# Performance work log

Hardware: AMD Instinct MI355X
Metric: run time of the kernel (lower is better)

Reference implementation:

```python
import jax, jax.numpy as jnp
import numpy as np

D = 128          # data_dim
H = 512          # hidden_dim
K = 10           # num_bins
BATCH = 32768
BOUND = 5.0
MINW = 1e-3
MINH = 1e-3
MIND = 1e-3
MASK = np.array([1.0] * (D // 2) + [0.0] * (D // 2), dtype=np.float32)
TIDX = np.where(MASK == 0)[0]  # transformed dims (static)


def _rqs_forward(x, uw, uh, ud):
    # x: [B, T]; uw/uh: [B, T, K]; ud: [B, T, K-1]
    w = jax.nn.softmax(uw, axis=-1)
    w = MINW + (1.0 - MINW * K) * w
    cw = jnp.pad(jnp.cumsum(w, axis=-1), ((0, 0), (0, 0), (1, 0)))
    cw = 2.0 * BOUND * cw - BOUND
    cw = cw.at[..., 0].set(-BOUND).at[..., -1].set(BOUND)
    w = cw[..., 1:] - cw[..., :-1]

    h = jax.nn.softmax(uh, axis=-1)
    h = MINH + (1.0 - MINH * K) * h
    ch = jnp.pad(jnp.cumsum(h, axis=-1), ((0, 0), (0, 0), (1, 0)))
    ch = 2.0 * BOUND * ch - BOUND
    ch = ch.at[..., 0].set(-BOUND).at[..., -1].set(BOUND)
    h = ch[..., 1:] - ch[..., :-1]

    d = MIND + jax.nn.softplus(ud)
    d = jnp.pad(d, ((0, 0), (0, 0), (1, 1)), constant_values=1.0)  # [B,T,K+1]

    inside = (x >= -BOUND) & (x <= BOUND)
    xc = jnp.clip(x, -BOUND, BOUND)  # avoid NaN for outside values

    # searchsorted(cw, x, right=True) - 1, clamped to [0, K-1]
    bin_idx = jnp.clip(jnp.sum(cw <= xc[..., None], axis=-1) - 1, 0, K - 1)

    def gat(a, idx):
        return jnp.take_along_axis(a, idx[..., None], axis=-1)[..., 0]

    wk = gat(w, bin_idx)
    cwk = gat(cw, bin_idx)
    hk = gat(h, bin_idx)
    chk = gat(ch, bin_idx)
    dk = gat(d, bin_idx)
    dk1 = gat(d, bin_idx + 1)

    theta = (xc - cwk) / wk
    s = hk / wk
    tm = theta * (1.0 - theta)
    den = s + (dk + dk1 - 2.0 * s) * tm
    num = hk * (s * theta * theta + dk * tm)
    y = chk + num / den
    ld = jnp.log(s * s * (dk1 * theta * theta + 2.0 * s * tm + dk * (1.0 - theta) ** 2)) - 2.0 * jnp.log(den)

    y = jnp.where(inside, y, x)
    ld = jnp.where(inside, ld, 0.0)
    return y, ld


def setup_inputs() -> dict:
    key = jax.random.key(0)
    ks = jax.random.split(key, 7)
    out_dim = D * (3 * K - 1)
    return {
        "z": jax.random.normal(ks[0], (BATCH, D), dtype=jnp.float32) * 2.0,
        "W1": jax.random.normal(ks[1], (H, D), dtype=jnp.float32) * 0.05,
        "b1": jnp.zeros((H,), dtype=jnp.float32),
        "W2": jax.random.normal(ks[2], (H, H), dtype=jnp.float32) * 0.05,
        "b2": jnp.zeros((H,), dtype=jnp.float32),
        "W3": jax.random.normal(ks[3], (out_dim, H), dtype=jnp.float32) * 0.05,
        "b3": jnp.zeros((out_dim,), dtype=jnp.float32),
    }


def reference(z, W1, b1, W2, b2, W3, b3):
    mask = jnp.asarray(MASK)
    z_a = z * mask
    hdn = jax.nn.relu(z_a @ W1.T + b1)
    hdn = jax.nn.relu(hdn @ W2.T + b2)
    p = (hdn @ W3.T + b3).reshape(-1, D, 3 * K - 1)
    uw, uh, ud = jnp.split(p, [K, 2 * K], axis=-1)

    zb = z[:, TIDX]
    xb, ld = _rqs_forward(zb, uw[:, TIDX], uh[:, TIDX], ud[:, TIDX])

    x = z.at[:, TIDX].set(xb)
    logdet = jnp.sum(ld, axis=1)
    x = jnp.where(jnp.isnan(x) | jnp.isinf(x), 0.0, x)
    logdet = jnp.where(jnp.isnan(logdet) | jnp.isinf(logdet), 0.0, logdet)
    return x, logdet
```

## Files before the change

### kernel.cpp

```cpp
#include <hip/hip_runtime.h>
#include <cmath>

#define BATCH 32768
#define DIM   128
#define HID   512
#define NPAD  2048

typedef __attribute__((ext_vector_type(8))) _Float16 half8;
typedef __attribute__((ext_vector_type(8))) short   short8v;
typedef __attribute__((ext_vector_type(4))) float   f32x4;
typedef unsigned short u16;


__device__ __forceinline__ u16 f2h(float f) {
  _Float16 h = (_Float16)f;
  union { _Float16 h; u16 u; } v; v.h = h; return v.u;
}

__device__ __forceinline__ void async16(const void* g, void* l) {
  __builtin_amdgcn_global_load_lds(
      (const __attribute__((address_space(1))) void*)g,
      (__attribute__((address_space(3))) void*)l, 16, 0, 0);
}

__device__ __forceinline__ int xcd_swz(int bid, int nwg) {
  int cpx = nwg >> 3;
  return (bid & 7) * cpx + (bid >> 3);
}


__global__ __launch_bounds__(256) void prep_za_v7(const float* __restrict__ z, u16* __restrict__ zh) {
  int id = blockIdx.x * 256 + threadIdx.x;
  int l = id & 63;
  int mb = (id >> 6) & 2047;
  int kt = id >> 17;
  int r = mb * 16 + (l & 15);
  int k0 = kt * 32 + ((l >> 4) << 3);
  const float* src = z + (size_t)r * DIM + k0;
  short8v H;
#pragma unroll
  for (int j = 0; j < 8; ++j) H[j] = (short)f2h(src[j]);
  *(short8v*)(zh + (size_t)id * 8) = H;
}

__global__ __launch_bounds__(256) void prep_w12_v7(const float* __restrict__ W1, const float* __restrict__ W2,
                                                   u16* __restrict__ W1h, u16* __restrict__ W2h) {
  int id = blockIdx.x * 256 + threadIdx.x;
  if (id < 4096) {
    int l = id & 63, mb = (id >> 6) & 31, kt = id >> 11;
    int r = mb * 16 + (l & 15);
    int k0 = kt * 32 + ((l >> 4) << 3);
    const float* src = W1 + (size_t)r * DIM + k0;
    short8v H;
#pragma unroll
    for (int j = 0; j < 8; ++j) H[j] = (short)f2h(src[j]);
    *(short8v*)(W1h + (size_t)id * 8) = H;
  } else {
    int id2 = id - 4096;
    int l = id2 & 63, mb = (id2 >> 6) & 31, kt = id2 >> 11;
    int r = mb * 16 + (l & 15);
    int k0 = kt * 32 + ((l >> 4) << 3);
    const float* src = W2 + (size_t)r * HID + k0;
    short8v H;
#pragma unroll
    for (int j = 0; j < 8; ++j) H[j] = (short)f2h(src[j]);
    *(short8v*)(W2h + (size_t)id2 * 8) = H;
  }
}

__global__ __launch_bounds__(256) void prep_w3_v7(const float* __restrict__ W3, u16* __restrict__ W3h) {
  int id = blockIdx.x * 256 + threadIdx.x;
  int l = id & 63, mb = (id >> 6) & 127, kt = id >> 13;
  int n = mb * 16 + (l & 15);
  int k0 = kt * 32 + ((l >> 4) << 3);
  int g = n >> 5, kk = n & 31;
  short8v H;
  if (kk < 29) {
    const float* src = W3 + ((size_t)((g + 64) * 29 + kk)) * HID + k0;
#pragma unroll
    for (int j = 0; j < 8; ++j) H[j] = (short)f2h(src[j]);
  } else {
#pragma unroll
    for (int j = 0; j < 8; ++j) H[j] = 0;
  }
  *(short8v*)(W3h + (size_t)id * 8) = H;
}

__global__ __launch_bounds__(256) void prep_b3_v7(const float* __restrict__ b3, float* __restrict__ b3p) {
  int n = blockIdx.x * 256 + threadIdx.x;
  int g = n >> 5, kk = n & 31;
  b3p[n] = (kk < 29) ? b3[(g + 64) * 29 + kk] : 0.f;
}


__device__ __forceinline__ void stage4(const u16* __restrict__ A, const u16* __restrict__ B,
                                       size_t ab, size_t bb, u16* Lb, int t) {
  async16(A + ab + t * 8,         Lb + t * 8);
  async16(A + ab + (t + 256) * 8, Lb + (t + 256) * 8);
  async16(B + bb + t * 8,         Lb + 4096 + t * 8);
  async16(B + bb + (t + 256) * 8, Lb + 4096 + (t + 256) * 8);
}

__device__ __forceinline__ void compute_v7(const u16* Lb, int lane, int wr, int wc, f32x4 acc[4][4]) {
  half8 a[4], b[4];
#pragma unroll
  for (int mf = 0; mf < 4; ++mf)
    a[mf] = *(const half8*)(Lb + ((wr * 4 + mf) * 64 + lane) * 8);
#pragma unroll
  for (int nf = 0; nf < 4; ++nf)
    b[nf] = *(const half8*)(Lb + 4096 + ((wc * 4 + nf) * 64 + lane) * 8);
#pragma unroll
  for (int mf = 0; mf < 4; ++mf)
#pragma unroll
    for (int nf = 0; nf < 4; ++nf)
      acc[mf][nf] = __builtin_amdgcn_mfma_f32_16x16x32_f16(a[mf], b[nf], acc[mf][nf], 0, 0, 0);
}

__device__ __forceinline__ void gemm_mainloop_v7(
    const u16* __restrict__ A, const u16* __restrict__ B,
    int nkt, int a_rb0, int a_rs16, int b_rb0, int b_rs16,
    u16* LDS, f32x4 acc[4][4]) {
  const int t = threadIdx.x;
  const int lane = t & 63;
  const int wv = t >> 6;
  const int wr = wv >> 1, wc = wv & 1;
  const size_t aStep = (size_t)a_rs16 * 512;
  const size_t bStep = (size_t)b_rs16 * 512;
  size_t ab = (size_t)a_rb0 * 512;
  size_t bb = (size_t)b_rb0 * 512;

  stage4(A, B, ab, bb, LDS, t);
  stage4(A, B, ab + aStep, bb + bStep, LDS + 8192, t);

  for (int kt = 0; kt < nkt; ++kt) {
    if (kt + 2 < nkt) {
      stage4(A, B, ab + 2 * aStep, bb + 2 * bStep, LDS + ((kt + 2) & 3) * 8192, t);
      asm volatile("s_waitcnt vmcnt(8)" ::: "memory");
    } else if (kt + 1 < nkt) {
      asm volatile("s_waitcnt vmcnt(4)" ::: "memory");
    } else {
      asm volatile("s_waitcnt vmcnt(0)" ::: "memory");
    }
    __builtin_amdgcn_s_barrier();
    __builtin_amdgcn_sched_barrier(0);
    compute_v7(LDS + (kt & 3) * 8192, lane, wr, wc, acc);
    ab += aStep; bb += bStep;
  }
}


__global__ __launch_bounds__(256) void gemm_relu_v7(
    const u16* __restrict__ A, const u16* __restrict__ B,
    const float* __restrict__ bias, u16* __restrict__ C,
    int nkt, int a_rs16) {
  __shared__ __align__(16) u16 LDS[32768];
  const int bid = xcd_swz(blockIdx.x, gridDim.x);
  const int nt = bid & 3;
  const int mt = bid >> 2;
  const int m0 = mt << 7, n0 = nt << 7;
  f32x4 zero = {0.f, 0.f, 0.f, 0.f};
  f32x4 acc[4][4];
#pragma unroll
  for (int i = 0; i < 4; ++i)
#pragma unroll
    for (int j = 0; j < 4; ++j) acc[i][j] = zero;

  gemm_mainloop_v7(A, B, nkt, m0 >> 4, a_rs16, n0 >> 4, 32, LDS, acc);

  const int lane = threadIdx.x & 63;
  const int wv = threadIdx.x >> 6;
  const int wr = wv >> 1, wc = wv & 1;
#pragma unroll
  for (int mf = 0; mf < 4; ++mf) {
#pragma unroll
    for (int nf = 0; nf < 4; ++nf) {
      int col = n0 + wc * 64 + nf * 16 + (lane & 15);
      float bv = bias[col];
#pragma unroll
      for (int r = 0; r < 4; ++r) {
        int row = m0 + wr * 64 + mf * 16 + (lane >> 4) * 4 + r;
        float v = fmaxf(acc[mf][nf][r] + bv, 0.f);
        int ktO = col >> 5, mbO = row >> 4;
        int lO = (row & 15) | (((col >> 3) & 3) << 4);
        int jO = col & 7;
        size_t off = (((size_t)ktO * (BATCH >> 4) + mbO) * 64 + lO) * 8 + jO;
        C[off] = f2h(v);
      }
    }
  }
}


__device__ __forceinline__ void rqs(float xin, const float uw[10], const float uh[10], const float ud9[9],
                                    float& yv, float& ldv) {
  float mw = uw[0];
#pragma unroll
  for (int i = 1; i < 10; ++i) mw = fmaxf(mw, uw[i]);
  float ew[10]; float sw = 0.f;
#pragma unroll
  for (int i = 0; i < 10; ++i) { ew[i] = __expf(uw[i] - mw); sw += ew[i]; }
  float invw = 0.99f / sw;
  float cw[11]; cw[0] = -5.f;
  {
    float run = 0.f;
#pragma unroll
    for (int i = 0; i < 10; ++i) { run += 0.001f + invw * ew[i]; cw[i + 1] = 10.f * run - 5.f; }
  }
  cw[10] = 5.f;
  float mh = uh[0];
#pragma unroll
  for (int i = 1; i < 10; ++i) mh = fmaxf(mh, uh[i]);
  float eh[10]; float sh = 0.f;
#pragma unroll
  for (int i = 0; i < 10; ++i) { eh[i] = __expf(uh[i] - mh); sh += eh[i]; }
  float invh = 0.99f / sh;
  float ch[11]; ch[0] = -5.f;
  {
    float run = 0.f;
#pragma unroll
    for (int i = 0; i < 10; ++i) { run += 0.001f + invh * eh[i]; ch[i + 1] = 10.f * run - 5.f; }
  }
  ch[10] = 5.f;
  float dv[11]; dv[0] = 1.f; dv[10] = 1.f;
#pragma unroll
  for (int i = 0; i < 9; ++i) {
    float x = ud9[i];
    float sp = fmaxf(x, 0.f) + __logf(1.f + __expf(-fabsf(x)));
    dv[i + 1] = 0.001f + sp;
  }

  float xc = fminf(fmaxf(xin, -5.f), 5.f);
  int b = 0;
#pragma unroll
  for (int j = 1; j <= 10; ++j) b += (cw[j] <= xc) ? 1 : 0;
  b = (b > 9) ? 9 : b;

  float wk = cw[1] - cw[0], cwk = cw[0], hk = ch[1] - ch[0], chk = ch[0], dk = dv[0], dk1 = dv[1];
#pragma unroll
  for (int j = 1; j < 10; ++j) {
    if (j == b) { wk = cw[j + 1] - cw[j]; cwk = cw[j]; hk = ch[j + 1] - ch[j]; chk = ch[j]; dk = dv[j]; dk1 = dv[j + 1]; }
  }

  float th = (xc - cwk) / wk;
  float sr = hk / wk;
  float omth = 1.f - th;
  float tm = th * omth;
  float den = sr + (dk + dk1 - 2.f * sr) * tm;
  float num = hk * (sr * th * th + dk * tm);
  float y = chk + num / den;
  float ld = __logf(sr * sr * (dk1 * th * th + 2.f * sr * tm + dk * omth * omth)) - 2.f * __logf(den);
  bool inside = (xin >= -5.f) && (xin <= 5.f);
  yv = inside ? y : xin;
  ldv = inside ? ld : 0.f;
  if (!isfinite(yv)) yv = 0.f;
}


__global__ __launch_bounds__(256) void gemm3_spline_v7(
    const u16* __restrict__ A, const u16* __restrict__ B,
    const float* __restrict__ b3p, const float* __restrict__ z,
    float* __restrict__ xout, float* __restrict__ partial) {
  __shared__ __align__(16) char SMEM[65536];
  u16* LDS = (u16*)SMEM;
  float (*PT)[135] = (float(*)[135])SMEM;
  const int bid = xcd_swz(blockIdx.x, gridDim.x);
  const int nt = bid & 15;
  const int mt = bid >> 4;
  const int m0 = mt << 7, n0 = nt << 7;
  f32x4 zero = {0.f, 0.f, 0.f, 0.f};
  f32x4 acc[4][4];
#pragma unroll
  for (int i = 0; i < 4; ++i)
#pragma unroll
    for (int j = 0; j < 4; ++j) acc[i][j] = zero;

  gemm_mainloop_v7(A, B, 16, m0 >> 4, BATCH >> 4, n0 >> 4, NPAD >> 4, LDS, acc);

  const int t = threadIdx.x;
  const int lane = t & 63;
  const int wv = t >> 6;
  const int wr = wv >> 1, wc = wv & 1;
  const int gb = n0 >> 5;

  for (int p = 0; p < 2; ++p) {
    __syncthreads();
    if (wr == p) {
#pragma unroll
      for (int mf = 0; mf < 4; ++mf)
#pragma unroll
        for (int nf = 0; nf < 4; ++nf)
#pragma unroll
          for (int r = 0; r < 4; ++r) {
            int cl = wc * 64 + nf * 16 + (lane & 15);
            PT[mf * 16 + (lane >> 4) * 4 + r][(cl >> 5) * 33 + (cl & 31)] = acc[mf][nf][r];
          }
    }
    __syncthreads();

    const int rl = t >> 2;
    const int g = t & 3;
    const int row = p * 64 + rl;
    const int grow = m0 + row;
    const float* pr = &PT[rl][g * 33];
    const float* bb = b3p + n0 + g * 32;
    float uw[10], uh[10], ud9[9];
#pragma unroll
    for (int i = 0; i < 10; ++i) uw[i] = pr[i] + bb[i];
#pragma unroll
    for (int i = 0; i < 10; ++i) uh[i] = pr[10 + i] + bb[10 + i];
#pragma unroll
    for (int i = 0; i < 9; ++i) ud9[i] = pr[20 + i] + bb[20 + i];

    float xin = z[(long)grow * DIM + 64 + gb + g];
    float yv, ldv;
    rqs(xin, uw, uh, ud9, yv, ldv);

    xout[(long)grow * DIM + 64 + gb + g] = yv;

    float s = ldv;
    s += __shfl_down(s, 1);
    s += __shfl_down(s, 2);
    if (g == 0) partial[(long)nt * BATCH + grow] = s;
  }
}


__global__ __launch_bounds__(256) void copy_first_v7(const float* __restrict__ z, float* __restrict__ xout) {
  int id = blockIdx.x * 256 + threadIdx.x;
  int m = id >> 4, c4 = id & 15;
  const float4 v = *(const float4*)(z + (long)m * DIM + c4 * 4);
  *(float4*)(xout + (long)m * DIM + c4 * 4) = v;
}

__global__ __launch_bounds__(256) void reduce_ld_v7(const float* __restrict__ partial, float* __restrict__ ldout) {
  int row = blockIdx.x * 256 + threadIdx.x;
  float s = 0.f;
#pragma unroll
  for (int i = 0; i < 16; ++i) s += partial[(long)i * BATCH + row];
  if (!isfinite(s)) s = 0.f;
  ldout[row] = s;
}


extern "C" void kernel_launch(void* const* d_in, const int* in_sizes, int n_in,
                              void* d_out, int out_size, void* d_ws, size_t ws_size,
                              hipStream_t stream) {
  const float* z  = (const float*)d_in[0];
  const float* W1 = (const float*)d_in[1];
  const float* b1 = (const float*)d_in[2];
  const float* W2 = (const float*)d_in[3];
  const float* b2 = (const float*)d_in[4];
  const float* W3 = (const float*)d_in[5];
  const float* b3 = (const float*)d_in[6];
  float* xout  = (float*)d_out;
  float* ldout = xout + (size_t)BATCH * DIM;

  char* ws = (char*)d_ws;
  u16* W1h = (u16*)ws;  ws += (size_t)512 * 64 * 2;
  u16* W2h = (u16*)ws;  ws += (size_t)512 * 512 * 2;
  u16* W3h = (u16*)ws;  ws += (size_t)NPAD * HID * 2;
  float* b3p = (float*)ws; ws += (size_t)NPAD * 4;
  u16* zah  = (u16*)ws;
  float* part = (float*)ws; ws += (size_t)BATCH * 64 * 2;
  u16* h1h = (u16*)ws;  ws += (size_t)BATCH * HID * 2;
  u16* h2h = (u16*)ws;  ws += (size_t)BATCH * HID * 2;

  prep_za_v7 <<<(2 * 2048 * 64) / 256, 256, 0, stream>>>(z, zah);
  prep_w12_v7<<<(4096 + 32768) / 256, 256, 0, stream>>>(W1, W2, W1h, W2h);
  prep_w3_v7 <<<(16 * 128 * 64) / 256, 256, 0, stream>>>(W3, W3h);
  prep_b3_v7 <<<NPAD / 256, 256, 0, stream>>>(b3, b3p);

  gemm_relu_v7<<<(BATCH / 128) * 4, 256, 0, stream>>>(zah, W1h, b1, h1h, 2, BATCH >> 4);
  gemm_relu_v7<<<(BATCH / 128) * 4, 256, 0, stream>>>(h1h, W2h, b2, h2h, 16, BATCH >> 4);
  gemm3_spline_v7<<<(BATCH / 128) * (NPAD / 128), 256, 0, stream>>>(h2h, W3h, b3p, z, xout, part);

  copy_first_v7<<<(BATCH * 16) / 256, 256, 0, stream>>>(z, xout);
  reduce_ld_v7<<<BATCH / 256, 256, 0, stream>>>(part, ldout);
}
```

Measured before the change: 182.6 us.

## Load GEMM B fragments directly to registers, halve LDS, merge prep kernels

```diff
diff --git a/kernel.cpp b/kernel.cpp
--- a/kernel.cpp
+++ b/kernel.cpp
@@ -29,96 +29,77 @@
 }
 
 
-__global__ __launch_bounds__(256) void prep_za_v7(const float* __restrict__ z, u16* __restrict__ zh) {
-  int id = blockIdx.x * 256 + threadIdx.x;
-  int l = id & 63;
-  int mb = (id >> 6) & 2047;
-  int kt = id >> 17;
-  int r = mb * 16 + (l & 15);
-  int k0 = kt * 32 + ((l >> 4) << 3);
-  const float* src = z + (size_t)r * DIM + k0;
-  short8v H;
-#pragma unroll
-  for (int j = 0; j < 8; ++j) H[j] = (short)f2h(src[j]);
-  *(short8v*)(zh + (size_t)id * 8) = H;
-}
-
-__global__ __launch_bounds__(256) void prep_w12_v7(const float* __restrict__ W1, const float* __restrict__ W2,
-                                                   u16* __restrict__ W1h, u16* __restrict__ W2h) {
-  int id = blockIdx.x * 256 + threadIdx.x;
-  if (id < 4096) {
-    int l = id & 63, mb = (id >> 6) & 31, kt = id >> 11;
+__global__ __launch_bounds__(256) void prep_all_v8(
+    const float* __restrict__ z, const float* __restrict__ W1, const float* __restrict__ W2,
+    const float* __restrict__ W3, const float* __restrict__ b3,
+    u16* __restrict__ zh, u16* __restrict__ W1h, u16* __restrict__ W2h,
+    u16* __restrict__ W3h, float* __restrict__ b3p) {
+  const int bid = blockIdx.x;
+  if (bid < 1024) {
+    int id = bid * 256 + threadIdx.x;
+    int l = id & 63, mb = (id >> 6) & 2047, kt = id >> 17;
     int r = mb * 16 + (l & 15);
     int k0 = kt * 32 + ((l >> 4) << 3);
-    const float* src = W1 + (size_t)r * DIM + k0;
+    const float* src = z + (size_t)r * DIM + k0;
     short8v H;
 #pragma unroll
     for (int j = 0; j < 8; ++j) H[j] = (short)f2h(src[j]);
-    *(short8v*)(W1h + (size_t)id * 8) = H;
+    *(short8v*)(zh + (size_t)id * 8) = H;
+  } else if (bid < 1168) {
+    int id = (bid - 1024) * 256 + threadIdx.x;
+    if (id < 4096) {
+      int l = id & 63, mb = (id >> 6) & 31, kt = id >> 11;
+      int r = mb * 16 + (l & 15);
+      int k0 = kt * 32 + ((l >> 4) << 3);
+      const float* src = W1 + (size_t)r * DIM + k0;
+      short8v H;
+#pragma unroll
+      for (int j = 0; j < 8; ++j) H[j] = (short)f2h(src[j]);
+      *(short8v*)(W1h + (size_t)id * 8) = H;
+    } else {
+      int id2 = id - 4096;
+      int l = id2 & 63, mb = (id2 >> 6) & 31, kt = id2 >> 11;
+      int r = mb * 16 + (l & 15);
+      int k0 = kt * 32 + ((l >> 4) << 3);
+      const float* src = W2 + (size_t)r * HID + k0;
+      short8v H;
+#pragma unroll
+      for (int j = 0; j < 8; ++j) H[j] = (short)f2h(src[j]);
+      *(short8v*)(W2h + (size_t)id2 * 8) = H;
+    }
+  } else if (bid < 1680) {
+    int id = (bid - 1168) * 256 + threadIdx.x;
+    int l = id & 63, mb = (id >> 6) & 127, kt = id >> 13;
+    int n = mb * 16 + (l & 15);
+    int k0 = kt * 32 + ((l >> 4) << 3);
+    int g = n >> 5, kk = n & 31;
+    short8v H;
+    if (kk < 29) {
+      const float* src = W3 + ((size_t)((g + 64) * 29 + kk)) * HID + k0;
+#pragma unroll
+      for (int j = 0; j < 8; ++j) H[j] = (short)f2h(src[j]);
+    } else {
+#pragma unroll
+      for (int j = 0; j < 8; ++j) H[j] = 0;
+    }
+    *(short8v*)(W3h + (size_t)id * 8) = H;
   } else {
-    int id2 = id - 4096;
-    int l = id2 & 63, mb = (id2 >> 6) & 31, kt = id2 >> 11;
-    int r = mb * 16 + (l & 15);
-    int k0 = kt * 32 + ((l >> 4) << 3);
-    const float* src = W2 + (size_t)r * HID + k0;
-    short8v H;
-#pragma unroll
-    for (int j = 0; j < 8; ++j) H[j] = (short)f2h(src[j]);
-    *(short8v*)(W2h + (size_t)id2 * 8) = H;
-  }
-}
-
-__global__ __launch_bounds__(256) void prep_w3_v7(const float* __restrict__ W3, u16* __restrict__ W3h) {
-  int id = blockIdx.x * 256 + threadIdx.x;
-  int l = id & 63, mb = (id >> 6) & 127, kt = id >> 13;
-  int n = mb * 16 + (l & 15);
-  int k0 = kt * 32 + ((l >> 4) << 3);
-  int g = n >> 5, kk = n & 31;
-  short8v H;
-  if (kk < 29) {
-    const float* src = W3 + ((size_t)((g + 64) * 29 + kk)) * HID + k0;
-#pragma unroll
-    for (int j = 0; j < 8; ++j) H[j] = (short)f2h(src[j]);
-  } else {
-#pragma unroll
-    for (int j = 0; j < 8; ++j) H[j] = 0;
-  }
-  *(short8v*)(W3h + (size_t)id * 8) = H;
-}
-
-__global__ __launch_bounds__(256) void prep_b3_v7(const float* __restrict__ b3, float* __restrict__ b3p) {
-  int n = blockIdx.x * 256 + threadIdx.x;
-  int g = n >> 5, kk = n & 31;
-  b3p[n] = (kk < 29) ? b3[(g + 64) * 29 + kk] : 0.f;
-}
-
-
-__device__ __forceinline__ void stage4(const u16* __restrict__ A, const u16* __restrict__ B,
-                                       size_t ab, size_t bb, u16* Lb, int t) {
+    int n = (bid - 1680) * 256 + threadIdx.x;
+    int g = n >> 5, kk = n & 31;
+    b3p[n] = (kk < 29) ? b3[(g + 64) * 29 + kk] : 0.f;
+  }
+}
+
+
+__device__ __forceinline__ void stageA_v8(const u16* __restrict__ A, size_t ab, u16* Lb, int t) {
   async16(A + ab + t * 8,         Lb + t * 8);
   async16(A + ab + (t + 256) * 8, Lb + (t + 256) * 8);
-  async16(B + bb + t * 8,         Lb + 4096 + t * 8);
-  async16(B + bb + (t + 256) * 8, Lb + 4096 + (t + 256) * 8);
-}
-
-__device__ __forceinline__ void compute_v7(const u16* Lb, int lane, int wr, int wc, f32x4 acc[4][4]) {
-  half8 a[4], b[4];
-#pragma unroll
-  for (int mf = 0; mf < 4; ++mf)
-    a[mf] = *(const half8*)(Lb + ((wr * 4 + mf) * 64 + lane) * 8);
-#pragma unroll
-  for (int nf = 0; nf < 4; ++nf)
-    b[nf] = *(const half8*)(Lb + 4096 + ((wc * 4 + nf) * 64 + lane) * 8);
-#pragma unroll
-  for (int mf = 0; mf < 4; ++mf)
-#pragma unroll
-    for (int nf = 0; nf < 4; ++nf)
-      acc[mf][nf] = __builtin_amdgcn_mfma_f32_16x16x32_f16(a[mf], b[nf], acc[mf][nf], 0, 0, 0);
-}
-
-__device__ __forceinline__ void gemm_mainloop_v7(
+}
+
+template<int NKT>
+__device__ __forceinline__ void gemm_mainloop_v8(
     const u16* __restrict__ A, const u16* __restrict__ B,
-    int nkt, int a_rb0, int a_rs16, int b_rb0, int b_rs16,
+    int a_rb0, int a_rs16, int b_rb0, int b_rs16,
     u16* LDS, f32x4 acc[4][4]) {
   const int t = threadIdx.x;
   const int lane = t & 63;
@@ -126,34 +107,48 @@
   const int wr = wv >> 1, wc = wv & 1;
   const size_t aStep = (size_t)a_rs16 * 512;
   const size_t bStep = (size_t)b_rs16 * 512;
-  size_t ab = (size_t)a_rb0 * 512;
-  size_t bb = (size_t)b_rb0 * 512;
-
-  stage4(A, B, ab, bb, LDS, t);
-  stage4(A, B, ab + aStep, bb + bStep, LDS + 8192, t);
-
-  for (int kt = 0; kt < nkt; ++kt) {
-    if (kt + 2 < nkt) {
-      stage4(A, B, ab + 2 * aStep, bb + 2 * bStep, LDS + ((kt + 2) & 3) * 8192, t);
-      asm volatile("s_waitcnt vmcnt(8)" ::: "memory");
-    } else if (kt + 1 < nkt) {
-      asm volatile("s_waitcnt vmcnt(4)" ::: "memory");
-    } else {
-      asm volatile("s_waitcnt vmcnt(0)" ::: "memory");
-    }
+  const size_t ab0 = (size_t)a_rb0 * 512;
+  const u16* Bbase = B + (((size_t)(b_rb0 + wc * 4)) * 64 + lane) * 8;
+
+  half8 breg[2][4];
+#pragma unroll
+  for (int nf = 0; nf < 4; ++nf)
+    breg[0][nf] = *(const half8*)(Bbase + nf * 512);
+  stageA_v8(A, ab0, LDS, t);
+  if (NKT > 1) stageA_v8(A, ab0 + aStep, LDS + 4096, t);
+
+#pragma unroll
+  for (int kt = 0; kt < NKT; ++kt) {
+    if (kt + 1 < NKT) {
+#pragma unroll
+      for (int nf = 0; nf < 4; ++nf)
+        breg[(kt + 1) & 1][nf] = *(const half8*)(Bbase + (size_t)(kt + 1) * bStep + nf * 512);
+    }
+    if (kt + 2 < NKT)
+      stageA_v8(A, ab0 + (size_t)(kt + 2) * aStep, LDS + ((kt + 2) & 3) * 4096, t);
+    if (kt + 2 < NKT)      asm volatile("s_waitcnt vmcnt(8)" ::: "memory");
+    else if (kt + 1 < NKT) asm volatile("s_waitcnt vmcnt(6)" ::: "memory");
+    else                   asm volatile("s_waitcnt vmcnt(0)" ::: "memory");
     __builtin_amdgcn_s_barrier();
     __builtin_amdgcn_sched_barrier(0);
-    compute_v7(LDS + (kt & 3) * 8192, lane, wr, wc, acc);
-    ab += aStep; bb += bStep;
-  }
-}
-
-
-__global__ __launch_bounds__(256) void gemm_relu_v7(
+    half8 a[4];
+#pragma unroll
+    for (int mf = 0; mf < 4; ++mf)
+      a[mf] = *(const half8*)(LDS + (kt & 3) * 4096 + ((wr * 4 + mf) * 64 + lane) * 8);
+#pragma unroll
+    for (int mf = 0; mf < 4; ++mf)
+#pragma unroll
+      for (int nf = 0; nf < 4; ++nf)
+        acc[mf][nf] = __builtin_amdgcn_mfma_f32_16x16x32_f16(a[mf], breg[kt & 1][nf], acc[mf][nf], 0, 0, 0);
+  }
+}
+
+
+template<int NKT>
+__global__ __launch_bounds__(256, 3) void gemm_relu_v8(
     const u16* __restrict__ A, const u16* __restrict__ B,
-    const float* __restrict__ bias, u16* __restrict__ C,
-    int nkt, int a_rs16) {
-  __shared__ __align__(16) u16 LDS[32768];
+    const float* __restrict__ bias, u16* __restrict__ C, int a_rs16) {
+  __shared__ __align__(16) u16 LDS[16384];
   const int bid = xcd_swz(blockIdx.x, gridDim.x);
   const int nt = bid & 3;
   const int mt = bid >> 2;
@@ -165,7 +160,7 @@
 #pragma unroll
     for (int j = 0; j < 4; ++j) acc[i][j] = zero;
 
-  gemm_mainloop_v7(A, B, nkt, m0 >> 4, a_rs16, n0 >> 4, 32, LDS, acc);
+  gemm_mainloop_v8<NKT>(A, B, m0 >> 4, a_rs16, n0 >> 4, 32, LDS, acc);
 
   const int lane = threadIdx.x & 63;
   const int wv = threadIdx.x >> 6;
@@ -256,13 +251,13 @@
 }
 
 
-__global__ __launch_bounds__(256) void gemm3_spline_v7(
+__global__ __launch_bounds__(256, 3) void gemm3_spline_v8(
     const u16* __restrict__ A, const u16* __restrict__ B,
     const float* __restrict__ b3p, const float* __restrict__ z,
     float* __restrict__ xout, float* __restrict__ partial) {
-  __shared__ __align__(16) char SMEM[65536];
+  __shared__ __align__(16) char SMEM[33792];
   u16* LDS = (u16*)SMEM;
-  float (*PT)[135] = (float(*)[135])SMEM;
+  float* PTf = (float*)SMEM;
   const int bid = xcd_swz(blockIdx.x, gridDim.x);
   const int nt = bid & 15;
   const int mt = bid >> 4;
@@ -274,7 +269,7 @@
 #pragma unroll
     for (int j = 0; j < 4; ++j) acc[i][j] = zero;
 
-  gemm_mainloop_v7(A, B, 16, m0 >> 4, BATCH >> 4, n0 >> 4, NPAD >> 4, LDS, acc);
+  gemm_mainloop_v8<16>(A, B, m0 >> 4, BATCH >> 4, n0 >> 4, NPAD >> 4, LDS, acc);
 
   const int t = threadIdx.x;
   const int lane = t & 63;
@@ -292,7 +287,8 @@
 #pragma unroll
           for (int r = 0; r < 4; ++r) {
             int cl = wc * 64 + nf * 16 + (lane & 15);
-            PT[mf * 16 + (lane >> 4) * 4 + r][(cl >> 5) * 33 + (cl & 31)] = acc[mf][nf][r];
+            int rowl = mf * 16 + (lane >> 4) * 4 + r;
+            PTf[rowl * 132 + (cl >> 5) * 33 + (cl & 31)] = acc[mf][nf][r];
           }
     }
     __syncthreads();
@@ -301,7 +297,7 @@
     const int g = t & 3;
     const int row = p * 64 + rl;
     const int grow = m0 + row;
-    const float* pr = &PT[rl][g * 33];
+    const float* pr = PTf + rl * 132 + g * 33;
     const float* bb = b3p + n0 + g * 32;
     float uw[10], uh[10], ud9[9];
 #pragma unroll
@@ -325,14 +321,14 @@
 }
 
 
-__global__ __launch_bounds__(256) void copy_first_v7(const float* __restrict__ z, float* __restrict__ xout) {
+__global__ __launch_bounds__(256) void copy_first_v8(const float* __restrict__ z, float* __restrict__ xout) {
   int id = blockIdx.x * 256 + threadIdx.x;
   int m = id >> 4, c4 = id & 15;
   const float4 v = *(const float4*)(z + (long)m * DIM + c4 * 4);
   *(float4*)(xout + (long)m * DIM + c4 * 4) = v;
 }
 
-__global__ __launch_bounds__(256) void reduce_ld_v7(const float* __restrict__ partial, float* __restrict__ ldout) {
+__global__ __launch_bounds__(256) void reduce_ld_v8(const float* __restrict__ partial, float* __restrict__ ldout) {
   int row = blockIdx.x * 256 + threadIdx.x;
   float s = 0.f;
 #pragma unroll
@@ -365,15 +361,12 @@
   u16* h1h = (u16*)ws;  ws += (size_t)BATCH * HID * 2;
   u16* h2h = (u16*)ws;  ws += (size_t)BATCH * HID * 2;
 
-  prep_za_v7 <<<(2 * 2048 * 64) / 256, 256, 0, stream>>>(z, zah);
-  prep_w12_v7<<<(4096 + 32768) / 256, 256, 0, stream>>>(W1, W2, W1h, W2h);
-  prep_w3_v7 <<<(16 * 128 * 64) / 256, 256, 0, stream>>>(W3, W3h);
-  prep_b3_v7 <<<NPAD / 256, 256, 0, stream>>>(b3, b3p);
-
-  gemm_relu_v7<<<(BATCH / 128) * 4, 256, 0, stream>>>(zah, W1h, b1, h1h, 2, BATCH >> 4);
-  gemm_relu_v7<<<(BATCH / 128) * 4, 256, 0, stream>>>(h1h, W2h, b2, h2h, 16, BATCH >> 4);
-  gemm3_spline_v7<<<(BATCH / 128) * (NPAD / 128), 256, 0, stream>>>(h2h, W3h, b3p, z, xout, part);
-
-  copy_first_v7<<<(BATCH * 16) / 256, 256, 0, stream>>>(z, xout);
-  reduce_ld_v7<<<BATCH / 256, 256, 0, stream>>>(part, ldout);
-}
+  prep_all_v8<<<1688, 256, 0, stream>>>(z, W1, W2, W3, b3, zah, W1h, W2h, W3h, b3p);
+
+  gemm_relu_v8<2><<<(BATCH / 128) * 4, 256, 0, stream>>>(zah, W1h, b1, h1h, BATCH >> 4);
+  gemm_relu_v8<16><<<(BATCH / 128) * 4, 256, 0, stream>>>(h1h, W2h, b2, h2h, BATCH >> 4);
+  gemm3_spline_v8<<<(BATCH / 128) * (NPAD / 128), 256, 0, stream>>>(h2h, W3h, b3p, z, xout, part);
+
+  copy_first_v8<<<(BATCH * 16) / 256, 256, 0, stream>>>(z, xout);
+  reduce_ld_v8<<<BATCH / 256, 256, 0, stream>>>(part, ldout);
+}
```

After: 150.5 us. 17.6% less time.
